# Optimization experiments

Hardware: AMD Instinct MI355X
Metric: run time of the kernel (lower is better)

Reference implementation:

```python
import jax, jax.numpy as jnp
import numpy as np

B, H, W, C = 32, 32, 32, 256


def setup_inputs() -> dict:
    key = jax.random.key(0)
    k1, k2 = jax.random.split(key)
    feats1 = jax.random.normal(k1, (B, H, W, C), dtype=jnp.float32)
    feats2 = jax.random.normal(k2, (B, H, W, C), dtype=jnp.float32)
    return {"feats1": feats1, "feats2": feats2}


def reference(feats1, feats2):
    # Training path of LocalFeatureLoss (trainflag=True)
    b, h, w, c = feats1.shape
    l = h * w
    q = feats1.reshape(b, l, c)  # queries: (B, l, C)
    p = feats2.reshape(b, l, c)  # preds:   (B, l, C)
    # M[b, a, j] = <p[b,a], q[b,j]>  == fm2 @ fm1.T per batch
    M = jnp.einsum('bac,bjc->baj', p, q)  # (B, l_pred, l_query)
    max1 = jnp.argmax(M, axis=1)  # (B, l_q): best pred index for each query token
    max2 = jnp.argmax(M, axis=2)  # (B, l_p): best query index for each pred token
    # mutual nearest-neighbor check: m[b, j] = max2[b, max1[b, j]]
    m = jnp.take_along_axis(max2, max1, axis=1)  # (B, l_q)
    valid = jnp.arange(l)[None, :] == m          # (B, l_q) bool
    # gather matched pred descriptors and compute per-pair similarity
    matched_p = jnp.take_along_axis(p, max1[..., None], axis=1)  # (B, l_q, C)
    sims = jnp.sum(q * matched_p, axis=-1)                        # (B, l_q)
    cnt = jnp.sum(valid, axis=1).astype(sims.dtype)               # (B,)
    # mean over mutual NN pairs (torch mean over idx1)
    similarity = jnp.sum(jnp.where(valid, sims, 0.0), axis=1) / jnp.maximum(cnt, 1.0)
    return similarity
```

## Files before the change

### kernel.cpp

```cpp
#include <hip/hip_runtime.h>
#include <hip/hip_bf16.h>

#define BATCH 32
#define L 1024
#define CD 256
#define NRT 16
#define NQT 32

typedef __bf16 bf16x8 __attribute__((ext_vector_type(8)));
typedef float  f32x4  __attribute__((ext_vector_type(4)));
typedef unsigned long long u64;

__device__ __forceinline__ unsigned int enc_f32(float f) {
    unsigned int u = __float_as_uint(f);
    return ((int)u < 0) ? ~u : (u | 0x80000000u);
}
__device__ __forceinline__ float dec_f32(unsigned int u) {
    u = (u & 0x80000000u) ? (u & 0x7FFFFFFFu) : ~u;
    return __uint_as_float(u);
}
__device__ __forceinline__ u64 pmax(u64 a, u64 b) { return a > b ? a : b; }
__device__ __forceinline__ bf16x8 cvt8(float4 a, float4 b) {
    bf16x8 o;
    o[0] = (__bf16)a.x; o[1] = (__bf16)a.y; o[2] = (__bf16)a.z; o[3] = (__bf16)a.w;
    o[4] = (__bf16)b.x; o[5] = (__bf16)b.y; o[6] = (__bf16)b.z; o[7] = (__bf16)b.w;
    return o;
}

__global__ void __launch_bounds__(256)
__attribute__((amdgpu_waves_per_eu(2)))
mm_argmax_kernel(
    const float* __restrict__ qg,
    const float* __restrict__ pg,
    u64* __restrict__ colpart,
    int* __restrict__ max2)
{
    __shared__ __bf16 sA[4 * 4096];
    __shared__ __bf16 sB[2][8192];
    __shared__ u64 sRow[2][64];

    const int tid = threadIdx.x;
    const int bid = blockIdx.x;
    const int b  = bid & 31;
    const int rt = bid >> 5;

    const int lane = tid & 63;
    const int w    = tid >> 6;
    const int wm   = w >> 1;
    const int wn   = w & 1;
    const int quad = lane >> 4;
    const int l16  = lane & 15;

    const float* pA = pg + ((size_t)b * L + rt * 64) * CD;
    const float* pQ = qg + (size_t)b * L * CD;

    #pragma unroll
    for (int pass = 0; pass < 2; ++pass) {
        float4 t[8];
        #pragma unroll
        for (int s = 0; s < 4; ++s) {
            const int sid = (pass * 4 + s) * 256 + tid;
            const int row = sid >> 5;
            const int ks  = (sid >> 3) & 3;
            const int sl  = sid & 7;
            const float* src = pA + row * CD + ks * 64 + ((sl ^ (row & 7)) << 3);
            t[2 * s]     = ((const float4*)src)[0];
            t[2 * s + 1] = ((const float4*)src)[1];
        }
        #pragma unroll
        for (int s = 0; s < 4; ++s) {
            const int sid = (pass * 4 + s) * 256 + tid;
            const int row = sid >> 5;
            const int ks  = (sid >> 3) & 3;
            const int sl  = sid & 7;
            *(bf16x8*)&sA[ks * 4096 + row * 64 + sl * 8] = cvt8(t[2 * s], t[2 * s + 1]);
        }
    }
    {
        float4 t[8];
        #pragma unroll
        for (int s = 0; s < 4; ++s) {
            const int sid  = s * 256 + tid;
            const int crow = sid >> 3;
            const int sl   = sid & 7;
            const float* src = pQ + (size_t)crow * CD + ((sl ^ (crow & 7)) << 3);
            t[2 * s]     = ((const float4*)src)[0];
            t[2 * s + 1] = ((const float4*)src)[1];
        }
        #pragma unroll
        for (int s = 0; s < 4; ++s) {
            const int sid  = s * 256 + tid;
            const int crow = sid >> 3;
            const int sl   = sid & 7;
            *(bf16x8*)&sB[0][crow * 64 + sl * 8] = cvt8(t[2 * s], t[2 * s + 1]);
        }
    }

    f32x4 acc[2][4];
    u64 rowbest[2][4];
    #pragma unroll
    for (int tm = 0; tm < 2; ++tm)
        #pragma unroll
        for (int r = 0; r < 4; ++r) rowbest[tm][r] = 0ull;

    const int a0q = rt * 64 + wm * 32 + quad * 4;
    const size_t colbase = ((size_t)b * 32 + rt * 2 + wm) * L;

    float4 pf[8];

    #pragma unroll 4
    for (int t = 0; t < NQT; ++t) {
        asm volatile("s_waitcnt lgkmcnt(0)" ::: "memory");
        __builtin_amdgcn_s_barrier();
        __builtin_amdgcn_sched_barrier(0);

        if (t < NQT - 1) {
            const int pos1 = (t + 1) >> 2, ks1 = (t + 1) & 3;
            #pragma unroll
            for (int s = 0; s < 4; ++s) {
                const int sid  = s * 256 + tid;
                const int crow = sid >> 3;
                const int sl   = sid & 7;
                const float* src = pQ + (size_t)(pos1 * 128 + crow) * CD
                                 + ks1 * 64 + ((sl ^ (crow & 7)) << 3);
                pf[2 * s]     = ((const float4*)src)[0];
                pf[2 * s + 1] = ((const float4*)src)[1];
            }
            __builtin_amdgcn_sched_barrier(0);
        }

        const int ks = t & 3;
        const __bf16* sBb = sB[t & 1];
        if (ks == 0) {
            #pragma unroll
            for (int tm = 0; tm < 2; ++tm)
                #pragma unroll
                for (int tn = 0; tn < 4; ++tn) acc[tm][tn] = (f32x4){0.f, 0.f, 0.f, 0.f};
        }
        __builtin_amdgcn_s_setprio(1);
        #pragma unroll
        for (int kk = 0; kk < 2; ++kk) {
            const int sw = ((kk * 4 + quad) ^ (l16 & 7)) << 3;
            bf16x8 a0 = *(const bf16x8*)&sA[ks * 4096 + (wm * 32      + l16) * 64 + sw];
            bf16x8 a1 = *(const bf16x8*)&sA[ks * 4096 + (wm * 32 + 16 + l16) * 64 + sw];
            bf16x8 b0 = *(const bf16x8*)&sBb[(wn * 64      + l16) * 64 + sw];
            bf16x8 b1 = *(const bf16x8*)&sBb[(wn * 64 + 16 + l16) * 64 + sw];
            bf16x8 b2 = *(const bf16x8*)&sBb[(wn * 64 + 32 + l16) * 64 + sw];
            bf16x8 b3 = *(const bf16x8*)&sBb[(wn * 64 + 48 + l16) * 64 + sw];
            acc[0][0] = __builtin_amdgcn_mfma_f32_16x16x32_bf16(a0, b0, acc[0][0], 0, 0, 0);
            acc[0][1] = __builtin_amdgcn_mfma_f32_16x16x32_bf16(a0, b1, acc[0][1], 0, 0, 0);
            acc[0][2] = __builtin_amdgcn_mfma_f32_16x16x32_bf16(a0, b2, acc[0][2], 0, 0, 0);
            acc[0][3] = __builtin_amdgcn_mfma_f32_16x16x32_bf16(a0, b3, acc[0][3], 0, 0, 0);
            acc[1][0] = __builtin_amdgcn_mfma_f32_16x16x32_bf16(a1, b0, acc[1][0], 0, 0, 0);
            acc[1][1] = __builtin_amdgcn_mfma_f32_16x16x32_bf16(a1, b1, acc[1][1], 0, 0, 0);
            acc[1][2] = __builtin_amdgcn_mfma_f32_16x16x32_bf16(a1, b2, acc[1][2], 0, 0, 0);
            acc[1][3] = __builtin_amdgcn_mfma_f32_16x16x32_bf16(a1, b3, acc[1][3], 0, 0, 0);
        }
        __builtin_amdgcn_s_setprio(0);
        __builtin_amdgcn_sched_barrier(0);

        if (t < NQT - 1) {
            #pragma unroll
            for (int s = 0; s < 4; ++s) {
                const int sid  = s * 256 + tid;
                const int crow = sid >> 3;
                const int sl   = sid & 7;
                *(bf16x8*)&sB[(t + 1) & 1][crow * 64 + sl * 8] =
                    cvt8(pf[2 * s], pf[2 * s + 1]);
            }
        }

        if (ks == 3) {
            const int pos = t >> 2;
            const int jb = pos * 128 + wn * 64 + l16;
            #pragma unroll
            for (int tm = 0; tm < 2; ++tm)
                #pragma unroll
                for (int r = 0; r < 4; ++r)
                    #pragma unroll
                    for (int tn = 0; tn < 4; ++tn) {
                        const u64 pk = ((u64)enc_f32(acc[tm][tn][r]) << 32)
                                     | (unsigned int)(~(unsigned int)(jb + tn * 16));
                        rowbest[tm][r] = pmax(rowbest[tm][r], pk);
                    }
            #pragma unroll
            for (int tn = 0; tn < 4; ++tn) {
                float cv = acc[0][tn][0];
                int   ca = a0q;
                #pragma unroll
                for (int tm = 0; tm < 2; ++tm)
                    #pragma unroll
                    for (int r = 0; r < 4; ++r) {
                        if (tm == 0 && r == 0) continue;
                        if (acc[tm][tn][r] > cv) { cv = acc[tm][tn][r]; ca = a0q + tm * 16 + r; }
                    }
                u64 pk = ((u64)enc_f32(cv) << 32) | (unsigned int)(~(unsigned int)ca);
                pk = pmax(pk, __shfl_xor(pk, 16));
                pk = pmax(pk, __shfl_xor(pk, 32));
                if (quad == 0)
                    colpart[colbase + pos * 128 + wn * 64 + tn * 16 + l16] = pk;
            }
        }
    }

    #pragma unroll
    for (int tm = 0; tm < 2; ++tm)
        #pragma unroll
        for (int r = 0; r < 4; ++r) {
            u64 pk = rowbest[tm][r];
            pk = pmax(pk, __shfl_xor(pk, 1));
            pk = pmax(pk, __shfl_xor(pk, 2));
            pk = pmax(pk, __shfl_xor(pk, 4));
            pk = pmax(pk, __shfl_xor(pk, 8));
            if (l16 == 0) sRow[wn][wm * 32 + tm * 16 + quad * 4 + r] = pk;
        }
    __syncthreads();
    if (tid < 64) {
        const u64 m = pmax(sRow[0][tid], sRow[1][tid]);
        max2[(size_t)b * L + rt * 64 + tid] = (int)(~(unsigned int)m) & (L - 1);
    }
}

__global__ __launch_bounds__(1024) void finalize_kernel(
    const u64* __restrict__ colpart,
    const int* __restrict__ max2,
    float* __restrict__ out)
{
    __shared__ int sMax2[L];
    __shared__ float sSum[16];
    __shared__ int sCnt[16];
    const int b = blockIdx.x;
    const int j = threadIdx.x;

    sMax2[j] = max2[(size_t)b * L + j];

    u64 cb = 0ull;
    #pragma unroll
    for (int k = 0; k < 32; ++k)
        cb = pmax(cb, colpart[((size_t)b * 32 + k) * L + j]);
    __syncthreads();

    const int a = (int)(~(unsigned int)cb) & (L - 1);
    const float val = dec_f32((unsigned int)(cb >> 32));
    const bool mut = (sMax2[a] == j);
    float sum = mut ? val : 0.f;
    int   cnt = mut ? 1 : 0;

    #pragma unroll
    for (int o = 32; o >= 1; o >>= 1) {
        sum += __shfl_down(sum, o);
        cnt += __shfl_down(cnt, o);
    }
    if ((j & 63) == 0) { sSum[j >> 6] = sum; sCnt[j >> 6] = cnt; }
    __syncthreads();
    if (j == 0) {
        float S = 0.f;
        int   C = 0;
        #pragma unroll
        for (int i = 0; i < 16; ++i) { S += sSum[i]; C += sCnt[i]; }
        out[b] = S / fmaxf((float)C, 1.0f);
    }
}

extern "C" void kernel_launch(void* const* d_in, const int* in_sizes, int n_in,
                              void* d_out, int out_size, void* d_ws, size_t ws_size,
                              hipStream_t stream) {
    const float* q = (const float*)d_in[0];
    const float* p = (const float*)d_in[1];
    float* out = (float*)d_out;

    u64* colpart = (u64*)d_ws;
    int* max2 = (int*)(colpart + (size_t)BATCH * 32 * L);

    mm_argmax_kernel<<<BATCH * NRT, 256, 0, stream>>>(q, p, colpart, max2);
    finalize_kernel<<<BATCH, 1024, 0, stream>>>(colpart, max2, out);
}
```

Measured before the change: 142.8 us.

## Pre-convert inputs to bf16 MFMA fragment layout and drop shared-memory staging

Adds a separate conversion kernel that turns both fp32 inputs into bf16 arrays already laid out in MFMA fragment order in workspace. The matmul-argmax kernel now runs 512 threads, keeps its A fragments in registers, and reads B fragments straight from global memory instead of staging through double-buffered LDS with barriers. This removes the per-tile fp32 reloads and conversion as well as LDS synchronisation. In exchange it adds an extra launch and a bf16 write and read pass over both inputs, and it relies on L2 to serve the repeated B reads, with no latency-hiding prefetch.

After: 153.1 us. 7.2% more time.

```diff
diff --git a/kernel.cpp b/kernel.cpp
--- a/kernel.cpp
+++ b/kernel.cpp
@@ -4,8 +4,6 @@
 #define BATCH 32
 #define L 1024
 #define CD 256
-#define NRT 16
-#define NQT 32
 
 typedef __bf16 bf16x8 __attribute__((ext_vector_type(8)));
 typedef float  f32x4  __attribute__((ext_vector_type(4)));
@@ -27,17 +25,45 @@
     return o;
 }
 
-__global__ void __launch_bounds__(256)
-__attribute__((amdgpu_waves_per_eu(2)))
-mm_argmax_kernel(
+__global__ __launch_bounds__(256) void convert_kernel(
     const float* __restrict__ qg,
     const float* __restrict__ pg,
+    __bf16* __restrict__ qT,
+    __bf16* __restrict__ pT)
+{
+    const unsigned int t = blockIdx.x * 256 + threadIdx.x;
+    const unsigned int v = t & 0xFFFFFu;
+    const int lane = v & 63;
+    const int l    = lane & 15;
+    const int q    = lane >> 4;
+    const float* src;
+    __bf16* dst;
+    if (t >> 20) {
+        const int kf = (v >> 6) & 7;
+        const int cf = (v >> 9) & 63;
+        const int b  = v >> 15;
+        src = qg + ((size_t)(b << 10) + (cf << 4) + l) * CD + (kf << 5) + (q << 3);
+        dst = qT + (size_t)v * 8;
+    } else {
+        const int f  = (v >> 6) & 15;
+        const int rw = (v >> 10) & 31;
+        const int b  = v >> 15;
+        const int row = (rw << 5) + ((f >> 3) << 4) + l;
+        src = pg + ((size_t)(b << 10) + row) * CD + ((f & 7) << 5) + (q << 3);
+        dst = pT + (size_t)v * 8;
+    }
+    const float4 f0 = ((const float4*)src)[0];
+    const float4 f1 = ((const float4*)src)[1];
+    *(bf16x8*)dst = cvt8(f0, f1);
+}
+
+__global__ __launch_bounds__(512) void mm_argmax_kernel(
+    const __bf16* __restrict__ qT,
+    const __bf16* __restrict__ pT,
     u64* __restrict__ colpart,
     int* __restrict__ max2)
 {
-    __shared__ __bf16 sA[4 * 4096];
-    __shared__ __bf16 sB[2][8192];
-    __shared__ u64 sRow[2][64];
+    __shared__ u64 sRow[4][64];
 
     const int tid = threadIdx.x;
     const int bid = blockIdx.x;
@@ -46,57 +72,20 @@
 
     const int lane = tid & 63;
     const int w    = tid >> 6;
-    const int wm   = w >> 1;
-    const int wn   = w & 1;
+    const int wm   = w >> 2;
+    const int wn   = w & 3;
     const int quad = lane >> 4;
     const int l16  = lane & 15;
 
-    const float* pA = pg + ((size_t)b * L + rt * 64) * CD;
-    const float* pQ = qg + (size_t)b * L * CD;
-
-    #pragma unroll
-    for (int pass = 0; pass < 2; ++pass) {
-        float4 t[8];
-        #pragma unroll
-        for (int s = 0; s < 4; ++s) {
-            const int sid = (pass * 4 + s) * 256 + tid;
-            const int row = sid >> 5;
-            const int ks  = (sid >> 3) & 3;
-            const int sl  = sid & 7;
-            const float* src = pA + row * CD + ks * 64 + ((sl ^ (row & 7)) << 3);
-            t[2 * s]     = ((const float4*)src)[0];
-            t[2 * s + 1] = ((const float4*)src)[1];
-        }
-        #pragma unroll
-        for (int s = 0; s < 4; ++s) {
-            const int sid = (pass * 4 + s) * 256 + tid;
-            const int row = sid >> 5;
-            const int ks  = (sid >> 3) & 3;
-            const int sl  = sid & 7;
-            *(bf16x8*)&sA[ks * 4096 + row * 64 + sl * 8] = cvt8(t[2 * s], t[2 * s + 1]);
-        }
-    }
-    {
-        float4 t[8];
-        #pragma unroll
-        for (int s = 0; s < 4; ++s) {
-            const int sid  = s * 256 + tid;
-            const int crow = sid >> 3;
-            const int sl   = sid & 7;
-            const float* src = pQ + (size_t)crow * CD + ((sl ^ (crow & 7)) << 3);
-            t[2 * s]     = ((const float4*)src)[0];
-            t[2 * s + 1] = ((const float4*)src)[1];
-        }
-        #pragma unroll
-        for (int s = 0; s < 4; ++s) {
-            const int sid  = s * 256 + tid;
-            const int crow = sid >> 3;
-            const int sl   = sid & 7;
-            *(bf16x8*)&sB[0][crow * 64 + sl * 8] = cvt8(t[2 * s], t[2 * s + 1]);
-        }
-    }
-
-    f32x4 acc[2][4];
+    const __bf16* pA = pT + (size_t)((b * 32 + rt * 2 + wm) * 16) * 512;
+    bf16x8 afr[16];
+    #pragma unroll
+    for (int f = 0; f < 16; ++f)
+        afr[f] = *(const bf16x8*)&pA[(size_t)(f * 64 + lane) * 8];
+
+    const __bf16* pB = qT + (size_t)b * (64 * 8 * 512);
+
+    f32x4 acc[2][2];
     u64 rowbest[2][4];
     #pragma unroll
     for (int tm = 0; tm < 2; ++tm)
@@ -106,100 +95,53 @@
     const int a0q = rt * 64 + wm * 32 + quad * 4;
     const size_t colbase = ((size_t)b * 32 + rt * 2 + wm) * L;
 
-    float4 pf[8];
-
-    #pragma unroll 4
-    for (int t = 0; t < NQT; ++t) {
-        asm volatile("s_waitcnt lgkmcnt(0)" ::: "memory");
-        __builtin_amdgcn_s_barrier();
-        __builtin_amdgcn_sched_barrier(0);
-
-        if (t < NQT - 1) {
-            const int pos1 = (t + 1) >> 2, ks1 = (t + 1) & 3;
+    for (int t = 0; t < 8; ++t) {
+        const int cf0 = wn * 16 + t * 2;
+        const __bf16* pBt = pB + (size_t)cf0 * (8 * 512);
+
+        #pragma unroll
+        for (int tm = 0; tm < 2; ++tm)
             #pragma unroll
-            for (int s = 0; s < 4; ++s) {
-                const int sid  = s * 256 + tid;
-                const int crow = sid >> 3;
-                const int sl   = sid & 7;
-                const float* src = pQ + (size_t)(pos1 * 128 + crow) * CD
-                                 + ks1 * 64 + ((sl ^ (crow & 7)) << 3);
-                pf[2 * s]     = ((const float4*)src)[0];
-                pf[2 * s + 1] = ((const float4*)src)[1];
-            }
-            __builtin_amdgcn_sched_barrier(0);
+            for (int tn = 0; tn < 2; ++tn) acc[tm][tn] = (f32x4){0.f, 0.f, 0.f, 0.f};
+
+        #pragma unroll
+        for (int kf = 0; kf < 8; ++kf) {
+            bf16x8 b0 = *(const bf16x8*)&pBt[(size_t)(kf * 64 + lane) * 8];
+            bf16x8 b1 = *(const bf16x8*)&pBt[(size_t)((8 + kf) * 64 + lane) * 8];
+            acc[0][0] = __builtin_amdgcn_mfma_f32_16x16x32_bf16(afr[kf],     b0, acc[0][0], 0, 0, 0);
+            acc[0][1] = __builtin_amdgcn_mfma_f32_16x16x32_bf16(afr[kf],     b1, acc[0][1], 0, 0, 0);
+            acc[1][0] = __builtin_amdgcn_mfma_f32_16x16x32_bf16(afr[8 + kf], b0, acc[1][0], 0, 0, 0);
+            acc[1][1] = __builtin_amdgcn_mfma_f32_16x16x32_bf16(afr[8 + kf], b1, acc[1][1], 0, 0, 0);
         }
 
-        const int ks = t & 3;
-        const __bf16* sBb = sB[t & 1];
-        if (ks == 0) {
+        const int jb = wn * 256 + t * 32 + l16;
+        #pragma unroll
+        for (int tm = 0; tm < 2; ++tm)
+            #pragma unroll
+            for (int r = 0; r < 4; ++r)
+                #pragma unroll
+                for (int tn = 0; tn < 2; ++tn) {
+                    const u64 pk = ((u64)enc_f32(acc[tm][tn][r]) << 32)
+                                 | (unsigned int)(~(unsigned int)(jb + tn * 16));
+                    rowbest[tm][r] = pmax(rowbest[tm][r], pk);
+                }
+
+        #pragma unroll
+        for (int tn = 0; tn < 2; ++tn) {
+            float cv = acc[0][tn][0];
+            int   ca = a0q;
             #pragma unroll
             for (int tm = 0; tm < 2; ++tm)
                 #pragma unroll
-                for (int tn = 0; tn < 4; ++tn) acc[tm][tn] = (f32x4){0.f, 0.f, 0.f, 0.f};
-        }
-        __builtin_amdgcn_s_setprio(1);
-        #pragma unroll
-        for (int kk = 0; kk < 2; ++kk) {
-            const int sw = ((kk * 4 + quad) ^ (l16 & 7)) << 3;
-            bf16x8 a0 = *(const bf16x8*)&sA[ks * 4096 + (wm * 32      + l16) * 64 + sw];
-            bf16x8 a1 = *(const bf16x8*)&sA[ks * 4096 + (wm * 32 + 16 + l16) * 64 + sw];
-            bf16x8 b0 = *(const bf16x8*)&sBb[(wn * 64      + l16) * 64 + sw];
-            bf16x8 b1 = *(const bf16x8*)&sBb[(wn * 64 + 16 + l16) * 64 + sw];
-            bf16x8 b2 = *(const bf16x8*)&sBb[(wn * 64 + 32 + l16) * 64 + sw];
-            bf16x8 b3 = *(const bf16x8*)&sBb[(wn * 64 + 48 + l16) * 64 + sw];
-            acc[0][0] = __builtin_amdgcn_mfma_f32_16x16x32_bf16(a0, b0, acc[0][0], 0, 0, 0);
-            acc[0][1] = __builtin_amdgcn_mfma_f32_16x16x32_bf16(a0, b1, acc[0][1], 0, 0, 0);
-            acc[0][2] = __builtin_amdgcn_mfma_f32_16x16x32_bf16(a0, b2, acc[0][2], 0, 0, 0);
-            acc[0][3] = __builtin_amdgcn_mfma_f32_16x16x32_bf16(a0, b3, acc[0][3], 0, 0, 0);
-            acc[1][0] = __builtin_amdgcn_mfma_f32_16x16x32_bf16(a1, b0, acc[1][0], 0, 0, 0);
-            acc[1][1] = __builtin_amdgcn_mfma_f32_16x16x32_bf16(a1, b1, acc[1][1], 0, 0, 0);
-            acc[1][2] = __builtin_amdgcn_mfma_f32_16x16x32_bf16(a1, b2, acc[1][2], 0, 0, 0);
-            acc[1][3] = __builtin_amdgcn_mfma_f32_16x16x32_bf16(a1, b3, acc[1][3], 0, 0, 0);
-        }
-        __builtin_amdgcn_s_setprio(0);
-        __builtin_amdgcn_sched_barrier(0);
-
-        if (t < NQT - 1) {
-            #pragma unroll
-            for (int s = 0; s < 4; ++s) {
-                const int sid  = s * 256 + tid;
-                const int crow = sid >> 3;
-                const int sl   = sid & 7;
-                *(bf16x8*)&sB[(t + 1) & 1][crow * 64 + sl * 8] =
-                    cvt8(pf[2 * s], pf[2 * s + 1]);
-            }
-        }
-
-        if (ks == 3) {
-            const int pos = t >> 2;
-            const int jb = pos * 128 + wn * 64 + l16;
-            #pragma unroll
-            for (int tm = 0; tm < 2; ++tm)
-                #pragma unroll
-                for (int r = 0; r < 4; ++r)
-                    #pragma unroll
-                    for (int tn = 0; tn < 4; ++tn) {
-                        const u64 pk = ((u64)enc_f32(acc[tm][tn][r]) << 32)
-                                     | (unsigned int)(~(unsigned int)(jb + tn * 16));
-                        rowbest[tm][r] = pmax(rowbest[tm][r], pk);
-                    }
-            #pragma unroll
-            for (int tn = 0; tn < 4; ++tn) {
-                float cv = acc[0][tn][0];
-                int   ca = a0q;
-                #pragma unroll
-                for (int tm = 0; tm < 2; ++tm)
-                    #pragma unroll
-                    for (int r = 0; r < 4; ++r) {
-                        if (tm == 0 && r == 0) continue;
-                        if (acc[tm][tn][r] > cv) { cv = acc[tm][tn][r]; ca = a0q + tm * 16 + r; }
-                    }
-                u64 pk = ((u64)enc_f32(cv) << 32) | (unsigned int)(~(unsigned int)ca);
-                pk = pmax(pk, __shfl_xor(pk, 16));
-                pk = pmax(pk, __shfl_xor(pk, 32));
-                if (quad == 0)
-                    colpart[colbase + pos * 128 + wn * 64 + tn * 16 + l16] = pk;
-            }
+                for (int r = 0; r < 4; ++r) {
+                    if (tm == 0 && r == 0) continue;
+                    if (acc[tm][tn][r] > cv) { cv = acc[tm][tn][r]; ca = a0q + tm * 16 + r; }
+                }
+            u64 pk = ((u64)enc_f32(cv) << 32) | (unsigned int)(~(unsigned int)ca);
+            pk = pmax(pk, __shfl_xor(pk, 16));
+            pk = pmax(pk, __shfl_xor(pk, 32));
+            if (quad == 0)
+                colpart[colbase + wn * 256 + t * 32 + tn * 16 + l16] = pk;
         }
     }
 
@@ -216,7 +158,8 @@
         }
     __syncthreads();
     if (tid < 64) {
-        const u64 m = pmax(sRow[0][tid], sRow[1][tid]);
+        const u64 m = pmax(pmax(sRow[0][tid], sRow[1][tid]),
+                           pmax(sRow[2][tid], sRow[3][tid]));
         max2[(size_t)b * L + rt * 64 + tid] = (int)(~(unsigned int)m) & (L - 1);
     }
 }
@@ -271,7 +214,10 @@
 
     u64* colpart = (u64*)d_ws;
     int* max2 = (int*)(colpart + (size_t)BATCH * 32 * L);
-
-    mm_argmax_kernel<<<BATCH * NRT, 256, 0, stream>>>(q, p, colpart, max2);
+    __bf16* pT = (__bf16*)((char*)d_ws + (8u << 20) + (512u << 10));
+    __bf16* qT = pT + (size_t)8388608;
+
+    convert_kernel<<<8192, 256, 0, stream>>>(q, p, qT, pT);
+    mm_argmax_kernel<<<BATCH * 16, 512, 0, stream>>>(qT, pT, colpart, max2);
     finalize_kernel<<<BATCH, 1024, 0, stream>>>(colpart, max2, out);
 }
```
